# Kernel optimization log

Measured on AMD Instinct MI355X. Metric: run time of the kernel, lower is better.

The kernel has to match this reference:

```python
import jax, jax.numpy as jnp
import numpy as np

TOP_K = 2


def setup_inputs() -> dict:
    key = jax.random.key(0)
    ks = jax.random.split(key, 9)
    T, D, E, F, FS = 8192, 2048, 8, 1024, 2048
    s = lambda k, shape, fan: jax.random.normal(k, shape, jnp.float32) * (fan ** -0.5)
    return {
        'hidden_states': jax.random.normal(ks[0], (T, D), jnp.float32),
        'gate_w': s(ks[1], (D, E), D),
        'w_gate': s(ks[2], (E, D, F), D),
        'w_up': s(ks[3], (E, D, F), D),
        'w_down': s(ks[4], (E, F, D), F),
        'ws_gate': s(ks[5], (D, FS), D),
        'ws_up': s(ks[6], (D, FS), D),
        'ws_down': s(ks[7], (FS, D), FS),
        'wsg': s(ks[8], (D, 1), D),
    }


def reference(hidden_states, gate_w, w_gate, w_up, w_down, ws_gate, ws_up, ws_down, wsg):
    E = gate_w.shape[1]
    h = hidden_states  # [T, D]
    # Router: softmax in fp32, top-k, normalized top-k probs
    logits = h @ gate_w  # [T, E]
    probs = jax.nn.softmax(logits.astype(jnp.float32), axis=-1)
    topk_w, topk_i = jax.lax.top_k(probs, TOP_K)  # [T, K]
    topk_w = topk_w / jnp.sum(topk_w, axis=-1, keepdims=True)
    topk_w = topk_w.astype(h.dtype)
    # Dense combine weights [T, E]: weight of expert e for each token (0 if not routed)
    comb = jnp.sum(jax.nn.one_hot(topk_i, E, dtype=topk_w.dtype) * topk_w[..., None], axis=1)
    # Per-expert gated MLP, weighted combine (zero weight == token not dispatched)
    out = jnp.zeros_like(h)
    for e in range(E):
        act = jax.nn.silu(h @ w_gate[e]) * (h @ w_up[e])  # [T, F]
        out = out + comb[:, e:e + 1] * (act @ w_down[e])
    # Shared expert with sigmoid gate
    shared = (jax.nn.silu(h @ ws_gate) * (h @ ws_up)) @ ws_down
    out = out + jax.nn.sigmoid(h @ wsg) * shared
    return out.astype(hidden_states.dtype)
```

## Files before the change

### kernel.cpp

```cpp
#include <hip/hip_runtime.h>
#include <hip/hip_bf16.h>

typedef short bf16x8 __attribute__((ext_vector_type(8)));
typedef float f32x4 __attribute__((ext_vector_type(4)));

__device__ __forceinline__ unsigned short f2b(float f) {
  union { float f; unsigned u; } v; v.f = f;
  unsigned r = v.u + 0x7FFF + ((v.u >> 16) & 1);
  return (unsigned short)(r >> 16);
}

__device__ __forceinline__ void async_b128(const void* g, void* l) {
  __builtin_amdgcn_global_load_lds(
      (const __attribute__((address_space(1))) unsigned int*)g,
      (__attribute__((address_space(3))) unsigned int*)l, 16, 0, 0);
}

__global__ void zero_f32_kernel(float* __restrict__ p, long n) {
  long i = (long)blockIdx.x * blockDim.x + threadIdx.x;
  long stride = (long)gridDim.x * blockDim.x;
  for (; i < n; i += stride) p[i] = 0.f;
}
__global__ void zero_i32_kernel(int* __restrict__ p, int n) {
  int i = blockIdx.x * blockDim.x + threadIdx.x;
  if (i < n) p[i] = 0;
}

__global__ __launch_bounds__(256) void convert_bf16_kernel(
    const float* __restrict__ src, unsigned short* __restrict__ dst, long n8) {
  long i = (long)blockIdx.x * blockDim.x + threadIdx.x;
  long stride = (long)gridDim.x * blockDim.x;
  for (; i < n8; i += stride) {
    const float* s = src + i * 8;
    float4 v0 = *(const float4*)s;
    float4 v1 = *(const float4*)(s + 4);
    bf16x8 w;
    w[0] = (short)f2b(v0.x); w[1] = (short)f2b(v0.y); w[2] = (short)f2b(v0.z); w[3] = (short)f2b(v0.w);
    w[4] = (short)f2b(v1.x); w[5] = (short)f2b(v1.y); w[6] = (short)f2b(v1.z); w[7] = (short)f2b(v1.w);
    *(bf16x8*)(dst + i * 8) = w;
  }
}

__global__ __launch_bounds__(256) void transpose_convert_kernel(
    const float* __restrict__ srcAll, unsigned short* __restrict__ dstAll,
    int R, int C) {
  const float* src = srcAll + (size_t)blockIdx.z * R * C;
  unsigned short* dst = dstAll + (size_t)blockIdx.z * R * C;
  int c0 = blockIdx.x * 64, r0 = blockIdx.y * 64;
  __shared__ float tile[64][73];
  int t = threadIdx.x;
  int sr = t >> 3;
  int sc = (t & 7) * 8;
#pragma unroll
  for (int rr = 0; rr < 2; ++rr) {
    int row = sr + rr * 32;
    const float* s = src + (size_t)(r0 + row) * C + c0 + sc;
    float4 v0 = *(const float4*)s;
    float4 v1 = *(const float4*)(s + 4);
    tile[row][sc + 0] = v0.x; tile[row][sc + 1] = v0.y;
    tile[row][sc + 2] = v0.z; tile[row][sc + 3] = v0.w;
    tile[row][sc + 4] = v1.x; tile[row][sc + 5] = v1.y;
    tile[row][sc + 6] = v1.z; tile[row][sc + 7] = v1.w;
  }
  __syncthreads();
#pragma unroll
  for (int pp = 0; pp < 2; ++pp) {
    int cc = sr + pp * 32;
    int rc = sc;
    bf16x8 w;
#pragma unroll
    for (int j = 0; j < 8; ++j) w[j] = (short)f2b(tile[rc + j][cc]);
    *(bf16x8*)(dst + (size_t)(c0 + cc) * R + r0 + rc) = w;
  }
}

__global__ __launch_bounds__(64) void router_kernel(
    const float* __restrict__ h, const float* __restrict__ gate_w,
    const float* __restrict__ wsg,
    int* __restrict__ cnt, int* __restrict__ slot_e, int* __restrict__ slot_pos,
    float* __restrict__ slot_w, float* __restrict__ gout, int D) {
  int t = blockIdx.x;
  int lane = threadIdx.x;
  float acc[8] = {0.f, 0.f, 0.f, 0.f, 0.f, 0.f, 0.f, 0.f};
  float aw = 0.f;
  const float* hrow = h + (size_t)t * D;
  for (int d = lane; d < D; d += 64) {
    float hv = hrow[d];
    float4 g0 = *(const float4*)(gate_w + (size_t)d * 8);
    float4 g1 = *(const float4*)(gate_w + (size_t)d * 8 + 4);
    acc[0] += hv * g0.x; acc[1] += hv * g0.y; acc[2] += hv * g0.z; acc[3] += hv * g0.w;
    acc[4] += hv * g1.x; acc[5] += hv * g1.y; acc[6] += hv * g1.z; acc[7] += hv * g1.w;
    aw += hv * wsg[d];
  }
#pragma unroll
  for (int off = 32; off > 0; off >>= 1) {
#pragma unroll
    for (int e = 0; e < 8; ++e) acc[e] += __shfl_down(acc[e], off);
    aw += __shfl_down(aw, off);
  }
  if (lane == 0) {
    int e0 = 0; float m0v = acc[0];
#pragma unroll
    for (int e = 1; e < 8; ++e) if (acc[e] > m0v) { m0v = acc[e]; e0 = e; }
    int e1 = -1; float m1v = -3.4e38f;
#pragma unroll
    for (int e = 0; e < 8; ++e) if (e != e0 && acc[e] > m1v) { m1v = acc[e]; e1 = e; }
    if (e1 < 0) e1 = (e0 + 1) & 7;
    float r = __expf(m1v - m0v);
    float w0 = 1.f / (1.f + r);
    float w1 = 1.f - w0;
    int p;
    p = atomicAdd(&cnt[e0], 1);
    slot_e[2 * t] = e0; slot_pos[2 * t] = p; slot_w[2 * t] = w0;
    p = atomicAdd(&cnt[e1], 1);
    slot_e[2 * t + 1] = e1; slot_pos[2 * t + 1] = p; slot_w[2 * t + 1] = w1;
    gout[t] = 1.f / (1.f + __expf(-aw));
  }
}

__global__ void scan_kernel(const int* __restrict__ cnt, int* __restrict__ offs, int E) {
  if (threadIdx.x == 0 && blockIdx.x == 0) {
    int s = 0;
    for (int e = 0; e < E; ++e) { offs[e] = s; s += cnt[e]; }
    offs[E] = s;
  }
}

__global__ void fill_kernel(const int* __restrict__ slot_e, const int* __restrict__ slot_pos,
                            const float* __restrict__ slot_w, const int* __restrict__ offs,
                            int* __restrict__ rowtok, float* __restrict__ roww, int n2T, int E) {
  int i = blockIdx.x * blockDim.x + threadIdx.x;
  if (i < n2T) {
    int e = slot_e[i];
    if (e < 0) e = 0; if (e >= E) e = E - 1;
    int row = offs[e] + slot_pos[i];
    if (row < 0) row = 0; if (row >= n2T) row = n2T - 1;
    rowtok[row] = i >> 1;
    roww[row] = slot_w[i];
  }
}

#define LDSOFF(row, kg) (((row) >> 3) * 512 + (kg) * 64 + ((row) & 7) * 8)

template <bool EXPERT, int K>
__global__ __launch_bounds__(256) void gemm_act3_kernel(
    const unsigned short* __restrict__ hb,
    const unsigned short* __restrict__ BgT,
    const unsigned short* __restrict__ BuT,
    unsigned short* __restrict__ actOut,
    const int* __restrict__ offs, const int* __restrict__ rowtok,
    int N, int rowsDirect, int T) {
  int e = EXPERT ? blockIdx.z : 0;
  int base = 0, cnt = rowsDirect;
  if (EXPERT) { base = offs[e]; cnt = offs[e + 1] - base; }
  int m0 = blockIdx.x * 128;
  if (m0 >= cnt) return;
  int n0 = blockIdx.y * 64;

  const unsigned short* Bg = BgT + (size_t)e * N * K;
  const unsigned short* Bu = BuT + (size_t)e * N * K;

  __shared__ __align__(16) unsigned short As[128 * 64];
  __shared__ __align__(16) unsigned short Bgs[64 * 64];
  __shared__ __align__(16) unsigned short Bus[64 * 64];

  int tid = threadIdx.x, lane = tid & 63, wave = tid >> 6;
  int r8 = lane & 7, kg = lane >> 3;
  int quad = lane >> 4, l16 = lane & 15;

  const unsigned short* aSrc[4];
#pragma unroll
  for (int t = 0; t < 4; ++t) {
    int gr = m0 + wave * 32 + t * 8 + r8;
    if (gr >= cnt) gr = cnt - 1;
    int tok = EXPERT ? rowtok[base + gr] : gr;
    if (tok < 0) tok = 0; if (tok >= T) tok = T - 1;
    aSrc[t] = hb + (size_t)tok * K + kg * 8;
  }
  const unsigned short* gSrc[2];
  const unsigned short* uSrc[2];
#pragma unroll
  for (int t = 0; t < 2; ++t) {
    int n = n0 + wave * 16 + t * 8 + r8;
    gSrc[t] = Bg + (size_t)n * K + kg * 8;
    uSrc[t] = Bu + (size_t)n * K + kg * 8;
  }
  unsigned short* aDst[4];
  unsigned short* gDst[2];
  unsigned short* uDst[2];
#pragma unroll
  for (int t = 0; t < 4; ++t) aDst[t] = As + (wave * 4 + t) * 512;
#pragma unroll
  for (int t = 0; t < 2; ++t) { gDst[t] = Bgs + (wave * 2 + t) * 512; uDst[t] = Bus + (wave * 2 + t) * 512; }

  f32x4 accG[2][4] = {};
  f32x4 accU[2][4] = {};

  for (int kt = 0; kt < K; kt += 64) {
#pragma unroll
    for (int t = 0; t < 4; ++t) async_b128(aSrc[t] + kt, aDst[t]);
#pragma unroll
    for (int t = 0; t < 2; ++t) { async_b128(gSrc[t] + kt, gDst[t]); async_b128(uSrc[t] + kt, uDst[t]); }
    __syncthreads();
#pragma unroll
    for (int ks = 0; ks < 2; ++ks) {
      int kq = ks * 4 + quad;
      bf16x8 a[2], bg[4], bu[4];
#pragma unroll
      for (int mi = 0; mi < 2; ++mi) {
        int m = wave * 32 + mi * 16 + l16;
        a[mi] = *(const bf16x8*)(As + LDSOFF(m, kq));
      }
#pragma unroll
      for (int nj = 0; nj < 4; ++nj) {
        int n = nj * 16 + l16;
        bg[nj] = *(const bf16x8*)(Bgs + LDSOFF(n, kq));
        bu[nj] = *(const bf16x8*)(Bus + LDSOFF(n, kq));
      }
#pragma unroll
      for (int mi = 0; mi < 2; ++mi)
#pragma unroll
        for (int nj = 0; nj < 4; ++nj) {
          accG[mi][nj] = __builtin_amdgcn_mfma_f32_16x16x32_bf16(a[mi], bg[nj], accG[mi][nj], 0, 0, 0);
          accU[mi][nj] = __builtin_amdgcn_mfma_f32_16x16x32_bf16(a[mi], bu[nj], accU[mi][nj], 0, 0, 0);
        }
    }
    __syncthreads();
  }

#pragma unroll
  for (int mi = 0; mi < 2; ++mi)
#pragma unroll
    for (int nj = 0; nj < 4; ++nj)
#pragma unroll
      for (int r = 0; r < 4; ++r) {
        int grow = m0 + wave * 32 + mi * 16 + quad * 4 + r;
        if (grow < cnt) {
          int col = n0 + nj * 16 + l16;
          float gv = accG[mi][nj][r], uv = accU[mi][nj][r];
          float sv = gv / (1.f + __expf(-gv)) * uv;
          actOut[(size_t)(base + grow) * N + col] = f2b(sv);
        }
      }
}

template <int MODE, int K>
__global__ __launch_bounds__(256) void gemm_comb3_kernel(
    const unsigned short* __restrict__ A,
    const unsigned short* __restrict__ BT,
    const int* __restrict__ offs, const int* __restrict__ rowtok,
    const float* __restrict__ roww, const float* __restrict__ gsig,
    float* __restrict__ out,
    int N, int rowsDirect, int T) {
  int e = (MODE == 0) ? blockIdx.z : 0;
  int base = 0, cnt = rowsDirect;
  if (MODE == 0) { base = offs[e]; cnt = offs[e + 1] - base; }
  int m0 = blockIdx.x * 128;
  if (m0 >= cnt) return;
  int n0 = blockIdx.y * 128;

  const unsigned short* B = BT + (size_t)e * N * K;

  __shared__ __align__(16) unsigned short As[128 * 64];
  __shared__ __align__(16) unsigned short Bs[128 * 64];

  int tid = threadIdx.x, lane = tid & 63, wave = tid >> 6;
  int r8 = lane & 7, kg = lane >> 3;
  int quad = lane >> 4, l16 = lane & 15;
  int mBase = (wave >> 1) * 64, nBase = (wave & 1) * 64;

  const unsigned short* aSrc[4];
  const unsigned short* bSrc[4];
#pragma unroll
  for (int t = 0; t < 4; ++t) {
    int gr = m0 + wave * 32 + t * 8 + r8;
    if (gr >= cnt) gr = cnt - 1;
    aSrc[t] = A + (size_t)(base + gr) * K + kg * 8;
    int n = n0 + wave * 32 + t * 8 + r8;
    bSrc[t] = B + (size_t)n * K + kg * 8;
  }
  unsigned short* aDst[4];
  unsigned short* bDst[4];
#pragma unroll
  for (int t = 0; t < 4; ++t) {
    aDst[t] = As + (wave * 4 + t) * 512;
    bDst[t] = Bs + (wave * 4 + t) * 512;
  }

  f32x4 acc[4][4] = {};

  for (int kt = 0; kt < K; kt += 64) {
#pragma unroll
    for (int t = 0; t < 4; ++t) { async_b128(aSrc[t] + kt, aDst[t]); async_b128(bSrc[t] + kt, bDst[t]); }
    __syncthreads();
#pragma unroll
    for (int ks = 0; ks < 2; ++ks) {
      int kq = ks * 4 + quad;
      bf16x8 a[4], b[4];
#pragma unroll
      for (int mi = 0; mi < 4; ++mi) {
        int m = mBase + mi * 16 + l16;
        a[mi] = *(const bf16x8*)(As + LDSOFF(m, kq));
      }
#pragma unroll
      for (int nj = 0; nj < 4; ++nj) {
        int n = nBase + nj * 16 + l16;
        b[nj] = *(const bf16x8*)(Bs + LDSOFF(n, kq));
      }
#pragma unroll
      for (int mi = 0; mi < 4; ++mi)
#pragma unroll
        for (int nj = 0; nj < 4; ++nj)
          acc[mi][nj] = __builtin_amdgcn_mfma_f32_16x16x32_bf16(a[mi], b[nj], acc[mi][nj], 0, 0, 0);
    }
    __syncthreads();
  }

#pragma unroll
  for (int mi = 0; mi < 4; ++mi)
#pragma unroll
    for (int nj = 0; nj < 4; ++nj)
#pragma unroll
      for (int r = 0; r < 4; ++r) {
        int grow = m0 + mBase + mi * 16 + quad * 4 + r;
        if (grow < cnt) {
          int col = n0 + nBase + nj * 16 + l16;
          float v = acc[mi][nj][r];
          if (MODE == 0) {
            int tok = rowtok[base + grow];
            if (tok < 0) tok = 0; if (tok >= T) tok = T - 1;
            atomicAdd(&out[(size_t)tok * N + col], roww[base + grow] * v);
          } else {
            out[(size_t)grow * N + col] += gsig[grow] * v;
          }
        }
      }
}

template <bool EXPERT>
__global__ __launch_bounds__(256) void gemm_act_f32_kernel(
    const float* __restrict__ X, const float* __restrict__ BgAll,
    const float* __restrict__ BuAll, unsigned short* __restrict__ actOut,
    const int* __restrict__ offs, const int* __restrict__ rowtok,
    int K, int N, int rowsDirect, int maxTok) {
  int e = EXPERT ? blockIdx.z : 0;
  int base = 0, cnt = rowsDirect;
  if (EXPERT) { base = offs[e]; cnt = offs[e + 1] - base; }
  int m0 = blockIdx.y * 64;
  if (m0 >= cnt) return;
  int n0 = blockIdx.x * 64;
  const float* Bg = BgAll + (size_t)e * K * N;
  const float* Bu = BuAll + (size_t)e * K * N;
  __shared__ __align__(16) short As[64][72];
  __shared__ __align__(16) short Bgs[64][72];
  __shared__ __align__(16) short Bus[64][72];
  int tid = threadIdx.x, lane = tid & 63, wave = tid >> 6;
  int quad = lane >> 4, l16 = lane & 15;
  int mBase = (wave >> 1) * 32, nBase = (wave & 1) * 32;
  f32x4 accG[2][2] = {};
  f32x4 accU[2][2] = {};
  int sr = tid >> 3, sc = (tid & 7) * 8;
  size_t aRowOff[2];
#pragma unroll
  for (int rr = 0; rr < 2; ++rr) {
    int gr = m0 + sr + rr * 32;
    if (gr >= cnt) gr = cnt - 1;
    int tokenRow = EXPERT ? rowtok[base + gr] : gr;
    if (tokenRow < 0) tokenRow = 0;
    if (tokenRow >= maxTok) tokenRow = maxTok - 1;
    aRowOff[rr] = (size_t)tokenRow * K;
  }
  for (int kt = 0; kt < K; kt += 64) {
#pragma unroll
    for (int rr = 0; rr < 2; ++rr) {
      int r = sr + rr * 32;
      const float* src = X + aRowOff[rr] + kt + sc;
      float4 v0 = *(const float4*)src;
      float4 v1 = *(const float4*)(src + 4);
      bf16x8 w;
      w[0] = (short)f2b(v0.x); w[1] = (short)f2b(v0.y); w[2] = (short)f2b(v0.z); w[3] = (short)f2b(v0.w);
      w[4] = (short)f2b(v1.x); w[5] = (short)f2b(v1.y); w[6] = (short)f2b(v1.z); w[7] = (short)f2b(v1.w);
      *(bf16x8*)&As[r][sc] = w;
    }
#pragma unroll
    for (int rr = 0; rr < 2; ++rr) {
      int kk = sr + rr * 32;
      const float* bg = Bg + (size_t)(kt + kk) * N + n0 + sc;
      const float* bu = Bu + (size_t)(kt + kk) * N + n0 + sc;
      float4 g0 = *(const float4*)bg; float4 g1 = *(const float4*)(bg + 4);
      float4 u0 = *(const float4*)bu; float4 u1 = *(const float4*)(bu + 4);
      Bgs[sc + 0][kk] = (short)f2b(g0.x); Bgs[sc + 1][kk] = (short)f2b(g0.y);
      Bgs[sc + 2][kk] = (short)f2b(g0.z); Bgs[sc + 3][kk] = (short)f2b(g0.w);
      Bgs[sc + 4][kk] = (short)f2b(g1.x); Bgs[sc + 5][kk] = (short)f2b(g1.y);
      Bgs[sc + 6][kk] = (short)f2b(g1.z); Bgs[sc + 7][kk] = (short)f2b(g1.w);
      Bus[sc + 0][kk] = (short)f2b(u0.x); Bus[sc + 1][kk] = (short)f2b(u0.y);
      Bus[sc + 2][kk] = (short)f2b(u0.z); Bus[sc + 3][kk] = (short)f2b(u0.w);
      Bus[sc + 4][kk] = (short)f2b(u1.x); Bus[sc + 5][kk] = (short)f2b(u1.y);
      Bus[sc + 6][kk] = (short)f2b(u1.z); Bus[sc + 7][kk] = (short)f2b(u1.w);
    }
    __syncthreads();
#pragma unroll
    for (int ks = 0; ks < 2; ++ks) {
      bf16x8 a[2], bg[2], bu[2];
#pragma unroll
      for (int i = 0; i < 2; ++i)
        a[i] = *(const bf16x8*)&As[mBase + i * 16 + l16][ks * 32 + quad * 8];
#pragma unroll
      for (int i = 0; i < 2; ++i) {
        bg[i] = *(const bf16x8*)&Bgs[nBase + i * 16 + l16][ks * 32 + quad * 8];
        bu[i] = *(const bf16x8*)&Bus[nBase + i * 16 + l16][ks * 32 + quad * 8];
      }
#pragma unroll
      for (int i = 0; i < 2; ++i)
#pragma unroll
        for (int j = 0; j < 2; ++j) {
          accG[i][j] = __builtin_amdgcn_mfma_f32_16x16x32_bf16(a[i], bg[j], accG[i][j], 0, 0, 0);
          accU[i][j] = __builtin_amdgcn_mfma_f32_16x16x32_bf16(a[i], bu[j], accU[i][j], 0, 0, 0);
        }
    }
    __syncthreads();
  }
#pragma unroll
  for (int i = 0; i < 2; ++i)
#pragma unroll
    for (int j = 0; j < 2; ++j)
#pragma unroll
      for (int r = 0; r < 4; ++r) {
        int row = mBase + i * 16 + quad * 4 + r;
        int grow = m0 + row;
        if (grow < cnt) {
          int col = n0 + nBase + j * 16 + l16;
          float gv = accG[i][j][r], uv = accU[i][j][r];
          float sv = gv / (1.f + __expf(-gv)) * uv;
          actOut[(size_t)(base + grow) * N + col] = f2b(sv);
        }
      }
}

template <int MODE>
__global__ __launch_bounds__(256) void gemm_comb_f32_kernel(
    const unsigned short* __restrict__ A, const float* __restrict__ BAll,
    const int* __restrict__ offs, const int* __restrict__ rowtok,
    const float* __restrict__ roww, float* __restrict__ accum,
    const float* __restrict__ gsig, float* __restrict__ out,
    int K, int N, int rowsDirect, int maxTok) {
  int e = (MODE == 0) ? blockIdx.z : 0;
  int base = 0, cnt = rowsDirect;
  if (MODE == 0) { base = offs[e]; cnt = offs[e + 1] - base; }
  int m0 = blockIdx.y * 64;
  if (m0 >= cnt) return;
  int n0 = blockIdx.x * 64;
  const float* B = BAll + (size_t)e * K * N;
  __shared__ __align__(16) short As[64][72];
  __shared__ __align__(16) short Bs[64][72];
  int tid = threadIdx.x, lane = tid & 63, wave = tid >> 6;
  int quad = lane >> 4, l16 = lane & 15;
  int mBase = (wave >> 1) * 32, nBase = (wave & 1) * 32;
  f32x4 acc[2][2] = {};
  int sr = tid >> 3, sc = (tid & 7) * 8;
  size_t aRowOff[2];
#pragma unroll
  for (int rr = 0; rr < 2; ++rr) {
    int gr = m0 + sr + rr * 32;
    if (gr >= cnt) gr = cnt - 1;
    aRowOff[rr] = (size_t)(base + gr) * K;
  }
  for (int kt = 0; kt < K; kt += 64) {
#pragma unroll
    for (int rr = 0; rr < 2; ++rr) {
      int r = sr + rr * 32;
      *(bf16x8*)&As[r][sc] = *(const bf16x8*)(A + aRowOff[rr] + kt + sc);
    }
#pragma unroll
    for (int rr = 0; rr < 2; ++rr) {
      int kk = sr + rr * 32;
      const float* bp = B + (size_t)(kt + kk) * N + n0 + sc;
      float4 b0 = *(const float4*)bp; float4 b1 = *(const float4*)(bp + 4);
      Bs[sc + 0][kk] = (short)f2b(b0.x); Bs[sc + 1][kk] = (short)f2b(b0.y);
      Bs[sc + 2][kk] = (short)f2b(b0.z); Bs[sc + 3][kk] = (short)f2b(b0.w);
      Bs[sc + 4][kk] = (short)f2b(b1.x); Bs[sc + 5][kk] = (short)f2b(b1.y);
      Bs[sc + 6][kk] = (short)f2b(b1.z); Bs[sc + 7][kk] = (short)f2b(b1.w);
    }
    __syncthreads();
#pragma unroll
    for (int ks = 0; ks < 2; ++ks) {
      bf16x8 a[2], b[2];
#pragma unroll
      for (int i = 0; i < 2; ++i)
        a[i] = *(const bf16x8*)&As[mBase + i * 16 + l16][ks * 32 + quad * 8];
#pragma unroll
      for (int i = 0; i < 2; ++i)
        b[i] = *(const bf16x8*)&Bs[nBase + i * 16 + l16][ks * 32 + quad * 8];
#pragma unroll
      for (int i = 0; i < 2; ++i)
#pragma unroll
        for (int j = 0; j < 2; ++j)
          acc[i][j] = __builtin_amdgcn_mfma_f32_16x16x32_bf16(a[i], b[j], acc[i][j], 0, 0, 0);
    }
    __syncthreads();
  }
#pragma unroll
  for (int i = 0; i < 2; ++i)
#pragma unroll
    for (int j = 0; j < 2; ++j)
#pragma unroll
      for (int r = 0; r < 4; ++r) {
        int row = mBase + i * 16 + quad * 4 + r;
        int grow = m0 + row;
        if (grow < cnt) {
          int col = n0 + nBase + j * 16 + l16;
          float v = acc[i][j][r];
          if (MODE == 0) {
            int tok = rowtok[base + grow];
            if (tok < 0) tok = 0;
            if (tok >= maxTok) tok = maxTok - 1;
            atomicAdd(&accum[(size_t)tok * N + col], roww[base + grow] * v);
          } else {
            out[(size_t)grow * N + col] = accum[(size_t)grow * N + col] + gsig[grow] * v;
          }
        }
      }
}

extern "C" void kernel_launch(void* const* d_in, const int* in_sizes, int n_in,
                              void* d_out, int out_size, void* d_ws, size_t ws_size,
                              hipStream_t stream) {
  const float* h       = (const float*)d_in[0];
  const float* gate_w  = (const float*)d_in[1];
  const float* w_gate  = (const float*)d_in[2];
  const float* w_up    = (const float*)d_in[3];
  const float* w_down  = (const float*)d_in[4];
  const float* ws_gate = (const float*)d_in[5];
  const float* ws_up   = (const float*)d_in[6];
  const float* ws_down = (const float*)d_in[7];
  const float* wsg     = (const float*)d_in[8];
  float* out = (float*)d_out;

  const int D  = in_sizes[8];
  const int T  = in_sizes[0] / D;
  const int E  = in_sizes[1] / D;
  const int F  = in_sizes[2] / (E * D);
  const int FS = in_sizes[5] / D;
  (void)n_in; (void)out_size;

  const int actPerTok = (2 * F > FS ? 2 * F : FS);

  size_t al = 256;
  auto rnd = [&](size_t b) { return (b + al - 1) & ~(al - 1); };
  size_t need = 0;
  need += rnd((size_t)T * D * 2);
  need += rnd((size_t)E * D * F * 2) * 3;
  need += rnd((size_t)D * FS * 2) * 3;
  need += rnd((size_t)T * actPerTok * 2);
  need += rnd((size_t)T * 4);
  need += rnd((size_t)E * 4) + rnd((size_t)(E + 1) * 4);
  need += rnd((size_t)2 * T * 4) * 5;

  bool shapeOK = (D == 2048 && F == 1024 && FS == 2048 && E == 8 && (T % 128) == 0);

  if (shapeOK && ws_size >= need) {
    char* ws = (char*)d_ws;
    size_t off = 0;
    auto alloc = [&](size_t bytes) -> void* { void* p = ws + off; off += rnd(bytes); return p; };
    unsigned short* hb   = (unsigned short*)alloc((size_t)T * D * 2);
    unsigned short* wgT  = (unsigned short*)alloc((size_t)E * D * F * 2);
    unsigned short* wuT  = (unsigned short*)alloc((size_t)E * D * F * 2);
    unsigned short* wdT  = (unsigned short*)alloc((size_t)E * D * F * 2);
    unsigned short* wsgT = (unsigned short*)alloc((size_t)D * FS * 2);
    unsigned short* wsuT = (unsigned short*)alloc((size_t)D * FS * 2);
    unsigned short* wsdT = (unsigned short*)alloc((size_t)D * FS * 2);
    unsigned short* act  = (unsigned short*)alloc((size_t)T * actPerTok * 2);
    float* g      = (float*)alloc((size_t)T * 4);
    int* cnt      = (int*)alloc((size_t)E * 4);
    int* offs     = (int*)alloc((size_t)(E + 1) * 4);
    int* slot_e   = (int*)alloc((size_t)2 * T * 4);
    int* slot_pos = (int*)alloc((size_t)2 * T * 4);
    float* slot_w = (float*)alloc((size_t)2 * T * 4);
    int* rowtok   = (int*)alloc((size_t)2 * T * 4);
    float* roww   = (float*)alloc((size_t)2 * T * 4);

    zero_i32_kernel<<<1, 64, 0, stream>>>(cnt, E);
    zero_f32_kernel<<<2048, 256, 0, stream>>>(out, (long)T * D);

    convert_bf16_kernel<<<2048, 256, 0, stream>>>(h, hb, (long)T * D / 8);
    transpose_convert_kernel<<<dim3(F / 64, D / 64, E), 256, 0, stream>>>(w_gate, wgT, D, F);
    transpose_convert_kernel<<<dim3(F / 64, D / 64, E), 256, 0, stream>>>(w_up, wuT, D, F);
    transpose_convert_kernel<<<dim3(D / 64, F / 64, E), 256, 0, stream>>>(w_down, wdT, F, D);
    transpose_convert_kernel<<<dim3(FS / 64, D / 64, 1), 256, 0, stream>>>(ws_gate, wsgT, D, FS);
    transpose_convert_kernel<<<dim3(FS / 64, D / 64, 1), 256, 0, stream>>>(ws_up, wsuT, D, FS);
    transpose_convert_kernel<<<dim3(D / 64, FS / 64, 1), 256, 0, stream>>>(ws_down, wsdT, FS, D);

    router_kernel<<<T, 64, 0, stream>>>(h, gate_w, wsg, cnt, slot_e, slot_pos, slot_w, g, D);
    scan_kernel<<<1, 64, 0, stream>>>(cnt, offs, E);
    fill_kernel<<<(2 * T + 255) / 256, 256, 0, stream>>>(slot_e, slot_pos, slot_w, offs,
                                                         rowtok, roww, 2 * T, E);

    int gxM = T / 128;
    gemm_act3_kernel<true, 2048><<<dim3(gxM, F / 64, E), 256, 0, stream>>>(
        hb, wgT, wuT, act, offs, rowtok, F, 0, T);
    gemm_comb3_kernel<0, 1024><<<dim3(gxM, D / 128, E), 256, 0, stream>>>(
        act, wdT, offs, rowtok, roww, nullptr, out, D, 0, T);
    gemm_act3_kernel<false, 2048><<<dim3(gxM, FS / 64, 1), 256, 0, stream>>>(
        hb, wsgT, wsuT, act, nullptr, nullptr, FS, T, T);
    gemm_comb3_kernel<1, 2048><<<dim3(gxM, D / 128, 1), 256, 0, stream>>>(
        act, wsdT, nullptr, nullptr, nullptr, g, out, D, T, T);
    return;
  }

  size_t perTok = (size_t)D * 4 + (size_t)actPerTok * 2 + 4 + 40;
  size_t avail = ws_size > 4096 ? ws_size - 4096 : 0;
  long TcL = (long)(avail / (perTok + 8));
  int Tc = (int)(TcL > T ? T : TcL);
  Tc &= ~63;
  if (Tc < 64) Tc = 64;

  for (int t0 = 0; t0 < T; t0 += Tc) {
    int Tcur = (T - t0 < Tc) ? (T - t0) : Tc;
    const float* hC = h + (size_t)t0 * D;
    float* outC = out + (size_t)t0 * D;

    char* ws = (char*)d_ws;
    size_t off = 0;
    auto alloc = [&](size_t bytes) -> void* { void* p = ws + off; off += rnd(bytes); return p; };
    float* accum = (float*)alloc((size_t)Tc * D * sizeof(float));
    unsigned short* act = (unsigned short*)alloc((size_t)Tc * actPerTok * 2);
    float* g      = (float*)alloc((size_t)Tc * 4);
    int* cnt      = (int*)alloc((size_t)E * 4);
    int* offs     = (int*)alloc((size_t)(E + 1) * 4);
    int* slot_e   = (int*)alloc((size_t)2 * Tc * 4);
    int* slot_pos = (int*)alloc((size_t)2 * Tc * 4);
    float* slot_w = (float*)alloc((size_t)2 * Tc * 4);
    int* rowtok   = (int*)alloc((size_t)2 * Tc * 4);
    float* roww   = (float*)alloc((size_t)2 * Tc * 4);

    int gy = (Tcur + 63) / 64;

    zero_i32_kernel<<<1, 64, 0, stream>>>(cnt, E);
    zero_f32_kernel<<<1024, 256, 0, stream>>>(accum, (long)Tcur * D);

    router_kernel<<<Tcur, 64, 0, stream>>>(hC, gate_w, wsg, cnt, slot_e, slot_pos, slot_w, g, D);
    scan_kernel<<<1, 64, 0, stream>>>(cnt, offs, E);
    fill_kernel<<<(2 * Tcur + 255) / 256, 256, 0, stream>>>(slot_e, slot_pos, slot_w, offs,
                                                            rowtok, roww, 2 * Tcur, E);
    gemm_act_f32_kernel<true><<<dim3(F / 64, gy, E), 256, 0, stream>>>(
        hC, w_gate, w_up, act, offs, rowtok, D, F, 0, Tcur);
    gemm_comb_f32_kernel<0><<<dim3(D / 64, gy, E), 256, 0, stream>>>(
        act, w_down, offs, rowtok, roww, accum, nullptr, nullptr, F, D, 0, Tcur);
    gemm_act_f32_kernel<false><<<dim3(FS / 64, gy, 1), 256, 0, stream>>>(
        hC, ws_gate, ws_up, act, nullptr, nullptr, D, FS, Tcur, Tcur);
    gemm_comb_f32_kernel<1><<<dim3(D / 64, gy, 1), 256, 0, stream>>>(
        act, ws_down, nullptr, nullptr, nullptr, accum, g, outC, FS, D, Tcur, Tcur);
  }
}
```

Measured before the change: 1.982 ms.

## Replace atomic scatter-add of expert outputs with bf16 gather in shared-expert epilogue

The expert down-projection no longer scatters into the fp32 output with atomicAdd. It writes per-slot results in bf16 into a buffer that reuses the gate-weight workspace. The shared-expert down-projection epilogue then gathers each token's two expert rows through a new token-to-row map and writes the final sum directly, so the output zeroing pass and the atomics go away. This costs extra bf16 rounding of expert outputs and adds gather reads in the last GEMM epilogue.

```diff
diff --git a/kernel.cpp b/kernel.cpp
--- a/kernel.cpp
+++ b/kernel.cpp
@@ -8,6 +8,11 @@
   union { float f; unsigned u; } v; v.f = f;
   unsigned r = v.u + 0x7FFF + ((v.u >> 16) & 1);
   return (unsigned short)(r >> 16);
+}
+
+__device__ __forceinline__ float b2f(unsigned short u) {
+  union { unsigned u; float f; } v; v.u = ((unsigned)u) << 16;
+  return v.f;
 }
 
 __device__ __forceinline__ void async_b128(const void* g, void* l) {
@@ -128,7 +133,8 @@
 
 __global__ void fill_kernel(const int* __restrict__ slot_e, const int* __restrict__ slot_pos,
                             const float* __restrict__ slot_w, const int* __restrict__ offs,
-                            int* __restrict__ rowtok, float* __restrict__ roww, int n2T, int E) {
+                            int* __restrict__ rowtok, float* __restrict__ roww,
+                            int* __restrict__ tokslot, int n2T, int E) {
   int i = blockIdx.x * blockDim.x + threadIdx.x;
   if (i < n2T) {
     int e = slot_e[i];
@@ -137,6 +143,7 @@
     if (row < 0) row = 0; if (row >= n2T) row = n2T - 1;
     rowtok[row] = i >> 1;
     roww[row] = slot_w[i];
+    tokslot[i] = row;
   }
 }
 
@@ -248,8 +255,12 @@
 __global__ __launch_bounds__(256) void gemm_comb3_kernel(
     const unsigned short* __restrict__ A,
     const unsigned short* __restrict__ BT,
-    const int* __restrict__ offs, const int* __restrict__ rowtok,
-    const float* __restrict__ roww, const float* __restrict__ gsig,
+    const int* __restrict__ offs,
+    const int* __restrict__ tokslot,
+    const float* __restrict__ slot_w,
+    const float* __restrict__ gsig,
+    const unsigned short* __restrict__ ye_in,
+    unsigned short* __restrict__ ye_out,
     float* __restrict__ out,
     int N, int rowsDirect, int T) {
   int e = (MODE == 0) ? blockIdx.z : 0;
@@ -319,22 +330,30 @@
 #pragma unroll
   for (int mi = 0; mi < 4; ++mi)
 #pragma unroll
-    for (int nj = 0; nj < 4; ++nj)
-#pragma unroll
-      for (int r = 0; r < 4; ++r) {
-        int grow = m0 + mBase + mi * 16 + quad * 4 + r;
-        if (grow < cnt) {
-          int col = n0 + nBase + nj * 16 + l16;
-          float v = acc[mi][nj][r];
-          if (MODE == 0) {
-            int tok = rowtok[base + grow];
-            if (tok < 0) tok = 0; if (tok >= T) tok = T - 1;
-            atomicAdd(&out[(size_t)tok * N + col], roww[base + grow] * v);
-          } else {
-            out[(size_t)grow * N + col] += gsig[grow] * v;
+    for (int r = 0; r < 4; ++r) {
+      int grow = m0 + mBase + mi * 16 + quad * 4 + r;
+      if (grow < cnt) {
+        if (MODE == 0) {
+#pragma unroll
+          for (int nj = 0; nj < 4; ++nj) {
+            int col = n0 + nBase + nj * 16 + l16;
+            ye_out[(size_t)(base + grow) * N + col] = f2b(acc[mi][nj][r]);
+          }
+        } else {
+          int r0 = tokslot[2 * grow], r1 = tokslot[2 * grow + 1];
+          float w0 = slot_w[2 * grow], w1 = slot_w[2 * grow + 1];
+          float gv = gsig[grow];
+#pragma unroll
+          for (int nj = 0; nj < 4; ++nj) {
+            int col = n0 + nBase + nj * 16 + l16;
+            float v = acc[mi][nj][r];
+            float e0 = b2f(ye_in[(size_t)r0 * N + col]);
+            float e1 = b2f(ye_in[(size_t)r1 * N + col]);
+            out[(size_t)grow * N + col] = gv * v + w0 * e0 + w1 * e1;
           }
         }
       }
+    }
 }
 
 template <bool EXPERT>
@@ -554,7 +573,7 @@
   need += rnd((size_t)T * actPerTok * 2);
   need += rnd((size_t)T * 4);
   need += rnd((size_t)E * 4) + rnd((size_t)(E + 1) * 4);
-  need += rnd((size_t)2 * T * 4) * 5;
+  need += rnd((size_t)2 * T * 4) * 6;
 
   bool shapeOK = (D == 2048 && F == 1024 && FS == 2048 && E == 8 && (T % 128) == 0);
 
@@ -578,9 +597,11 @@
     float* slot_w = (float*)alloc((size_t)2 * T * 4);
     int* rowtok   = (int*)alloc((size_t)2 * T * 4);
     float* roww   = (float*)alloc((size_t)2 * T * 4);
+    int* tokslot  = (int*)alloc((size_t)2 * T * 4);
+
+    unsigned short* ye = wgT;
 
     zero_i32_kernel<<<1, 64, 0, stream>>>(cnt, E);
-    zero_f32_kernel<<<2048, 256, 0, stream>>>(out, (long)T * D);
 
     convert_bf16_kernel<<<2048, 256, 0, stream>>>(h, hb, (long)T * D / 8);
     transpose_convert_kernel<<<dim3(F / 64, D / 64, E), 256, 0, stream>>>(w_gate, wgT, D, F);
@@ -593,21 +614,21 @@
     router_kernel<<<T, 64, 0, stream>>>(h, gate_w, wsg, cnt, slot_e, slot_pos, slot_w, g, D);
     scan_kernel<<<1, 64, 0, stream>>>(cnt, offs, E);
     fill_kernel<<<(2 * T + 255) / 256, 256, 0, stream>>>(slot_e, slot_pos, slot_w, offs,
-                                                         rowtok, roww, 2 * T, E);
+                                                         rowtok, roww, tokslot, 2 * T, E);
 
     int gxM = T / 128;
     gemm_act3_kernel<true, 2048><<<dim3(gxM, F / 64, E), 256, 0, stream>>>(
         hb, wgT, wuT, act, offs, rowtok, F, 0, T);
     gemm_comb3_kernel<0, 1024><<<dim3(gxM, D / 128, E), 256, 0, stream>>>(
-        act, wdT, offs, rowtok, roww, nullptr, out, D, 0, T);
+        act, wdT, offs, nullptr, nullptr, nullptr, nullptr, ye, nullptr, D, 0, T);
     gemm_act3_kernel<false, 2048><<<dim3(gxM, FS / 64, 1), 256, 0, stream>>>(
         hb, wsgT, wsuT, act, nullptr, nullptr, FS, T, T);
     gemm_comb3_kernel<1, 2048><<<dim3(gxM, D / 128, 1), 256, 0, stream>>>(
-        act, wsdT, nullptr, nullptr, nullptr, g, out, D, T, T);
+        act, wsdT, nullptr, tokslot, slot_w, g, ye, nullptr, out, D, T, T);
     return;
   }
 
-  size_t perTok = (size_t)D * 4 + (size_t)actPerTok * 2 + 4 + 40;
+  size_t perTok = (size_t)D * 4 + (size_t)actPerTok * 2 + 4 + 48;
   size_t avail = ws_size > 4096 ? ws_size - 4096 : 0;
   long TcL = (long)(avail / (perTok + 8));
   int Tc = (int)(TcL > T ? T : TcL);
@@ -632,6 +653,7 @@
     float* slot_w = (float*)alloc((size_t)2 * Tc * 4);
     int* rowtok   = (int*)alloc((size_t)2 * Tc * 4);
     float* roww   = (float*)alloc((size_t)2 * Tc * 4);
+    int* tokslot  = (int*)alloc((size_t)2 * Tc * 4);
 
     int gy = (Tcur + 63) / 64;
 
@@ -641,7 +663,7 @@
     router_kernel<<<Tcur, 64, 0, stream>>>(hC, gate_w, wsg, cnt, slot_e, slot_pos, slot_w, g, D);
     scan_kernel<<<1, 64, 0, stream>>>(cnt, offs, E);
     fill_kernel<<<(2 * Tcur + 255) / 256, 256, 0, stream>>>(slot_e, slot_pos, slot_w, offs,
-                                                            rowtok, roww, 2 * Tcur, E);
+                                                            rowtok, roww, tokslot, 2 * Tcur, E);
     gemm_act_f32_kernel<true><<<dim3(F / 64, gy, E), 256, 0, stream>>>(
         hC, w_gate, w_up, act, offs, rowtok, D, F, 0, Tcur);
     gemm_comb_f32_kernel<0><<<dim3(D / 64, gy, E), 256, 0, stream>>>(
```

Measured after the change: 1.682 ms. 1.18x faster.
